# Performance work log

Hardware: AMD Instinct MI355X
Metric: run time of the kernel (lower is better)

Reference implementation:

```python
import jax, jax.numpy as jnp
import numpy as np

NUM_SAMPLES = 4_194_304  # 2**22 samples (~87s @ 48kHz) -> memory-bound streaming IIR


def setup_inputs() -> dict:
    key = jax.random.key(0)
    k1, k2 = jax.random.split(key)
    # [attack, decay, filter_lp, filter_hp, gain]; uniform(0,1) is in the valid clamped range
    parameters = jax.random.uniform(k1, (5,), dtype=jnp.float32)
    noise = jax.random.normal(k2, (NUM_SAMPLES,), dtype=jnp.float32)
    return {"parameters": parameters, "noise": noise}


def _one_pole_lowpass(x, c):
    # y[n] = (1 - c) * x[n] + c * y[n-1]
    def step(y_prev, xn):
        y = (1.0 - c) * xn + c * y_prev
        return y, y
    _, y = jax.lax.scan(step, jnp.zeros((), x.dtype), x)
    return y


def _one_pole_highpass(x, c):
    # y[n] = c * (y[n-1] + x[n] - x[n-1])
    dx = jnp.concatenate([x[:1], x[1:] - x[:-1]])
    def step(y_prev, d):
        y = c * (y_prev + d)
        return y, y
    _, y = jax.lax.scan(step, jnp.zeros((), x.dtype), dx)
    return y


def reference(parameters, noise):
    attack = jnp.clip(parameters[0], 1e-7, None)
    decay = jnp.clip(parameters[1], 1e-7, None)
    filter_lp = jnp.clip(parameters[2], 1e-7, 0.99)
    filter_hp = jnp.clip(parameters[3], 1e-7, 0.99)
    gain = jnp.clip(parameters[4], 1e-7, None)

    n = noise.shape[0]
    t = jnp.linspace(0.0, 1.0, n, dtype=noise.dtype)  # matches registered 'time' buffer
    # exponential attack/decay envelope
    envelope = (1.0 - jnp.exp(-t / attack)) * jnp.exp(-t / decay)

    filtered = _one_pole_lowpass(noise, filter_lp)
    filtered = _one_pole_highpass(filtered, filter_hp)
    return filtered * envelope * gain
```

## Files before the change

kernel.cpp:

```cpp
#include <hip/hip_runtime.h>
#include <math.h>


#define BLOCK 256
#define CHUNK 20
#define HALO  1280
#define TWORDS (BLOCK * CHUNK)
#define SAMP   (TWORDS - HALO)

typedef float vfloat4 __attribute__((ext_vector_type(4)));

struct Op { float a, w, b; };
__device__ __forceinline__ Op opmul(Op A, Op B) {
    Op C;
    C.a = A.a * B.a;
    C.w = fmaf(A.w, B.a, A.b * B.w);
    C.b = A.b * B.b;
    return C;
}

__global__ __launch_bounds__(BLOCK) void ng_halo(
    const float* __restrict__ params,
    const float* __restrict__ noise,
    float* __restrict__ out, int n)
{
    __shared__ float swy[4], swz[4];

    const int tid  = threadIdx.x;
    const int lane = tid & 63;
    const int wid  = tid >> 6;
    const int base = blockIdx.x * SAMP - HALO;
    const int g0   = base + tid * CHUNK;

    const float a   = fminf(fmaxf(params[2], 1e-7f), 0.99f);
    const float bb  = fminf(fmaxf(params[3], 1e-7f), 0.99f);
    const float omc = 1.0f - a;

    vfloat4 xq[5];
    if (g0 >= 0 && g0 + CHUNK <= n) {
        #pragma unroll
        for (int q = 0; q < 5; ++q)
            xq[q] = *(const vfloat4*)(noise + g0 + 4 * q);
    } else {
        #pragma unroll
        for (int q = 0; q < 5; ++q) {
            #pragma unroll
            for (int c = 0; c < 4; ++c) {
                int g = g0 + 4 * q + c;
                xq[q][c] = (g >= 0 && g < n) ? noise[g] : 0.0f;
            }
        }
    }

    float yv = 0.0f, zv = 0.0f;
    #pragma unroll
    for (int j = 0; j < CHUNK; ++j) {
        float x  = xq[j >> 2][j & 3];
        float yn = fmaf(a, yv, omc * x);
        zv = bb * (zv + (yn - yv));
        yv = yn;
        xq[j >> 2][j & 3] = zv;
    }

    Op m1 = { a, bb * (a - 1.0f), bb };
    Op m2 = opmul(m1, m1), m4 = opmul(m2, m2), m8 = opmul(m4, m4), m16 = opmul(m8, m8);
    Op P  = opmul(m16, m4);
    Op O  = { 1.0f, 0.0f, 1.0f };
    float cy = yv, cz = zv;
    #pragma unroll
    for (int k = 0; k < 6; ++k) {
        if ((lane >> k) & 1) O = opmul(P, O);
        int d = 1 << k;
        float py = __shfl_up(cy, d, 64);
        float pz = __shfl_up(cz, d, 64);
        if (lane >= d) {
            cy = fmaf(P.a, py, cy);
            cz = fmaf(P.w, py, fmaf(P.b, pz, cz));
        }
        P = opmul(P, P);
    }
    if (lane == 63) { swy[wid] = cy; swz[wid] = cz; }

    float ey = __shfl_up(cy, 1, 64);
    float ez = __shfl_up(cz, 1, 64);
    if (lane == 0) { ey = 0.0f; ez = 0.0f; }

    __syncthreads();

    if (tid < HALO / CHUNK) return;

    float pry = 0.0f, prz = 0.0f;
    for (int u = 0; u < wid; ++u) {
        float ny = fmaf(P.a, pry, swy[u]);
        float nz = fmaf(P.w, pry, fmaf(P.b, prz, swz[u]));
        pry = ny; prz = nz;
    }

    float yh = fmaf(O.a, pry, ey);
    float zh = ez + fmaf(O.w, pry, O.b * prz);

    const float attack = fmaxf(params[0], 1e-7f);
    const float decay  = fmaxf(params[1], 1e-7f);
    const float gain   = fmaxf(params[4], 1e-7f);
    const float inv    = 1.0f / (float)(n - 1);
    const float ia = -1.0f / attack;
    const float id = -1.0f / decay;
    const float t0 = (float)g0 * inv;
    float ea = __expf(ia * t0);
    float ed = __expf(id * t0) * gain;
    const float ra = __expf(ia * inv);
    const float rd = __expf(id * inv);

    #pragma unroll
    for (int j = 0; j < CHUNK; ++j) {
        float yn = a * yh;
        zh = bb * (zh + (yn - yh));
        yh = yn;
        float zt = xq[j >> 2][j & 3] + zh;
        xq[j >> 2][j & 3] = zt * ((1.0f - ea) * ed);
        ea *= ra; ed *= rd;
    }

    if (g0 + CHUNK <= n) {
        #pragma unroll
        for (int q = 0; q < 5; ++q)
            __builtin_nontemporal_store(xq[q], (vfloat4*)(out + g0 + 4 * q));
    } else {
        #pragma unroll
        for (int q = 0; q < 5; ++q) {
            #pragma unroll
            for (int c = 0; c < 4; ++c) {
                int g = g0 + 4 * q + c;
                if (g < n) out[g] = xq[q][c];
            }
        }
    }
}

extern "C" void kernel_launch(void* const* d_in, const int* in_sizes, int n_in,
                              void* d_out, int out_size, void* d_ws, size_t ws_size,
                              hipStream_t stream) {
    const float* params = (const float*)d_in[0];
    const float* noise  = (const float*)d_in[1];
    float* out = (float*)d_out;
    int n = in_sizes[1];
    int grid = (n + SAMP - 1) / SAMP;
    ng_halo<<<grid, BLOCK, 0, stream>>>(params, noise, out, n);
}
```

Baseline: 84.82 us.

## Stage input and output through LDS for coalesced global loads and stores

Instead of each thread loading and storing its own 20-float contiguous chunk straight from global memory (strided across lanes), the block cooperatively loads the whole tile into shared memory with lane-contiguous float4 accesses, then each thread reads its chunk from LDS. Results go back to LDS and are written out coalesced with nontemporal stores. This targets poor coalescing of the 80-byte per-thread strides. In exchange it adds 20KB of LDS per block, two extra barriers and LDS traffic, and the halo warp now stays alive through the epilogue barrier.

```diff
diff --git a/kernel.cpp b/kernel.cpp
--- a/kernel.cpp
+++ b/kernel.cpp
@@ -19,38 +19,45 @@
     return C;
 }
 
-__global__ __launch_bounds__(BLOCK) void ng_halo(
+__global__ __launch_bounds__(BLOCK) void ng_r8(
     const float* __restrict__ params,
     const float* __restrict__ noise,
     float* __restrict__ out, int n)
 {
+    __shared__ __align__(16) float xs[TWORDS];
     __shared__ float swy[4], swz[4];
 
     const int tid  = threadIdx.x;
     const int lane = tid & 63;
     const int wid  = tid >> 6;
-    const int base = blockIdx.x * SAMP - HALO;
-    const int g0   = base + tid * CHUNK;
+    const int B    = blockIdx.x * SAMP;
+    const int base = B - HALO;
 
     const float a   = fminf(fmaxf(params[2], 1e-7f), 0.99f);
     const float bb  = fminf(fmaxf(params[3], 1e-7f), 0.99f);
     const float omc = 1.0f - a;
 
+    for (int v = tid; v < (TWORDS >> 2); v += BLOCK) {
+        int i = v << 2;
+        int g = base + i;
+        vfloat4 val;
+        if (g >= 0 && g + 4 <= n) {
+            val = *(const vfloat4*)(noise + g);
+        } else {
+            val.x = (g     >= 0 && g     < n) ? noise[g]     : 0.0f;
+            val.y = (g + 1 >= 0 && g + 1 < n) ? noise[g + 1] : 0.0f;
+            val.z = (g + 2 >= 0 && g + 2 < n) ? noise[g + 2] : 0.0f;
+            val.w = (g + 3 >= 0 && g + 3 < n) ? noise[g + 3] : 0.0f;
+        }
+        *(vfloat4*)(xs + i) = val;
+    }
+    __syncthreads();
+
+    const int l0 = tid * CHUNK;
     vfloat4 xq[5];
-    if (g0 >= 0 && g0 + CHUNK <= n) {
-        #pragma unroll
-        for (int q = 0; q < 5; ++q)
-            xq[q] = *(const vfloat4*)(noise + g0 + 4 * q);
-    } else {
-        #pragma unroll
-        for (int q = 0; q < 5; ++q) {
-            #pragma unroll
-            for (int c = 0; c < 4; ++c) {
-                int g = g0 + 4 * q + c;
-                xq[q][c] = (g >= 0 && g < n) ? noise[g] : 0.0f;
-            }
-        }
-    }
+    #pragma unroll
+    for (int q = 0; q < 5; ++q)
+        xq[q] = *(const vfloat4*)(xs + l0 + 4 * q);
 
     float yv = 0.0f, zv = 0.0f;
     #pragma unroll
@@ -87,52 +94,53 @@
 
     __syncthreads();
 
-    if (tid < HALO / CHUNK) return;
+    if (wid > 0) {
+        float pry = 0.0f, prz = 0.0f;
+        for (int u = 0; u < wid; ++u) {
+            float ny = fmaf(P.a, pry, swy[u]);
+            float nz = fmaf(P.w, pry, fmaf(P.b, prz, swz[u]));
+            pry = ny; prz = nz;
+        }
+        float yh = fmaf(O.a, pry, ey);
+        float zh = ez + fmaf(O.w, pry, O.b * prz);
 
-    float pry = 0.0f, prz = 0.0f;
-    for (int u = 0; u < wid; ++u) {
-        float ny = fmaf(P.a, pry, swy[u]);
-        float nz = fmaf(P.w, pry, fmaf(P.b, prz, swz[u]));
-        pry = ny; prz = nz;
-    }
+        const float attack = fmaxf(params[0], 1e-7f);
+        const float decay  = fmaxf(params[1], 1e-7f);
+        const float gain   = fmaxf(params[4], 1e-7f);
+        const float inv    = 1.0f / (float)(n - 1);
+        const float ia = -1.0f / attack;
+        const float id = -1.0f / decay;
+        const float t0 = (float)(base + l0) * inv;
+        float ea = __expf(ia * t0);
+        float ed = __expf(id * t0) * gain;
+        const float ra = __expf(ia * inv);
+        const float rd = __expf(id * inv);
 
-    float yh = fmaf(O.a, pry, ey);
-    float zh = ez + fmaf(O.w, pry, O.b * prz);
+        #pragma unroll
+        for (int j = 0; j < CHUNK; ++j) {
+            float yn = a * yh;
+            zh = bb * (zh + (yn - yh));
+            yh = yn;
+            float zt = xq[j >> 2][j & 3] + zh;
+            xq[j >> 2][j & 3] = zt * ((1.0f - ea) * ed);
+            ea *= ra; ed *= rd;
+        }
 
-    const float attack = fmaxf(params[0], 1e-7f);
-    const float decay  = fmaxf(params[1], 1e-7f);
-    const float gain   = fmaxf(params[4], 1e-7f);
-    const float inv    = 1.0f / (float)(n - 1);
-    const float ia = -1.0f / attack;
-    const float id = -1.0f / decay;
-    const float t0 = (float)g0 * inv;
-    float ea = __expf(ia * t0);
-    float ed = __expf(id * t0) * gain;
-    const float ra = __expf(ia * inv);
-    const float rd = __expf(id * inv);
-
-    #pragma unroll
-    for (int j = 0; j < CHUNK; ++j) {
-        float yn = a * yh;
-        zh = bb * (zh + (yn - yh));
-        yh = yn;
-        float zt = xq[j >> 2][j & 3] + zh;
-        xq[j >> 2][j & 3] = zt * ((1.0f - ea) * ed);
-        ea *= ra; ed *= rd;
-    }
-
-    if (g0 + CHUNK <= n) {
         #pragma unroll
         for (int q = 0; q < 5; ++q)
-            __builtin_nontemporal_store(xq[q], (vfloat4*)(out + g0 + 4 * q));
-    } else {
-        #pragma unroll
-        for (int q = 0; q < 5; ++q) {
-            #pragma unroll
-            for (int c = 0; c < 4; ++c) {
-                int g = g0 + 4 * q + c;
-                if (g < n) out[g] = xq[q][c];
-            }
+            *(vfloat4*)(xs + l0 + 4 * q) = xq[q];
+    }
+    __syncthreads();
+
+    for (int v = tid; v < (SAMP >> 2); v += BLOCK) {
+        int i = v << 2;
+        int g = B + i;
+        if (g + 4 <= n) {
+            vfloat4 val = *(const vfloat4*)(xs + HALO + i);
+            __builtin_nontemporal_store(val, (vfloat4*)(out + g));
+        } else {
+            for (int c = 0; c < 4; ++c)
+                if (g + c < n) out[g + c] = xs[HALO + i + c];
         }
     }
 }
@@ -145,5 +153,5 @@
     float* out = (float*)d_out;
     int n = in_sizes[1];
     int grid = (n + SAMP - 1) / SAMP;
-    ng_halo<<<grid, BLOCK, 0, stream>>>(params, noise, out, n);
+    ng_r8<<<grid, BLOCK, 0, stream>>>(params, noise, out, n);
 }
```

Result: faster. 74.80 us (-11.8%).
